# Kernel optimization log

Hardware: AMD Instinct MI355X
Metric: run time of the kernel (lower is better)

Reference implementation:

```python
import jax, jax.numpy as jnp
import numpy as np

N, T, D = 1536, 10, 64
H = 4            # nhead
HD = D // H      # head dim
EPS = 1e-5


def _ln(x, g, b):
    m = x.mean(-1, keepdims=True)
    v = ((x - m) ** 2).mean(-1, keepdims=True)
    return (x - m) / jnp.sqrt(v + EPS) * g + b


def setup_inputs() -> dict:
    key = jax.random.key(0)
    ks = jax.random.split(key, 24)
    s = 0.05
    inp = {
        'trajectories': jax.random.normal(ks[0], (N, T, D), jnp.float32),
        'adj_matrix': jax.random.uniform(ks[1], (N, N), jnp.float32),
        # transformer encoder layer params
        'attn_in_w': jax.random.normal(ks[2], (3 * D, D), jnp.float32) * s,
        'attn_in_b': jnp.zeros((3 * D,), jnp.float32),
        'attn_out_w': jax.random.normal(ks[3], (D, D), jnp.float32) * s,
        'attn_out_b': jnp.zeros((D,), jnp.float32),
        'ln1_g': jnp.ones((D,), jnp.float32),
        'ln1_b': jnp.zeros((D,), jnp.float32),
        'ff_w1': jax.random.normal(ks[4], (64, D), jnp.float32) * s,
        'ff_b1': jnp.zeros((64,), jnp.float32),
        'ff_w2': jax.random.normal(ks[5], (D, 64), jnp.float32) * s,
        'ff_b2': jnp.zeros((D,), jnp.float32),
        'ln2_g': jnp.ones((D,), jnp.float32),
        'ln2_b': jnp.zeros((D,), jnp.float32),
        # 3 GCN layers (hidden 64 -> 64)
        'gcn_w': jax.random.normal(ks[6], (3, 64, 64), jnp.float32) * s,
        'gcn_b': jnp.zeros((3, 64), jnp.float32),
        # edge predictor MLP: (2*64 + T) -> 128 -> 64 -> 1
        'e_w1': jax.random.normal(ks[7], (128, 2 * 64 + T), jnp.float32) * s,
        'e_b1': jnp.zeros((128,), jnp.float32),
        'e_w2': jax.random.normal(ks[8], (64, 128), jnp.float32) * s,
        'e_b2': jnp.zeros((64,), jnp.float32),
        'e_w3': jax.random.normal(ks[9], (1, 64), jnp.float32) * s,
        'e_b3': jnp.zeros((1,), jnp.float32),
    }
    return inp


def reference(trajectories, adj_matrix, attn_in_w, attn_in_b, attn_out_w,
              attn_out_b, ln1_g, ln1_b, ff_w1, ff_b1, ff_w2, ff_b2, ln2_g,
              ln2_b, gcn_w, gcn_b, e_w1, e_b1, e_w2, e_b2, e_w3, e_b3):
    x = trajectories  # (N,T,D)
    # --- torch TransformerEncoderLayer (post-norm, relu, eval mode) ---
    qkv = x @ attn_in_w.T + attn_in_b            # (N,T,3D)
    q, k, v = jnp.split(qkv, 3, axis=-1)
    q = q.reshape(N, T, H, HD)
    k = k.reshape(N, T, H, HD)
    v = v.reshape(N, T, H, HD)
    scores = jnp.einsum('nthd,nshd->nhts', q, k) / jnp.sqrt(jnp.float32(HD))
    attn = jax.nn.softmax(scores, axis=-1)
    ctx = jnp.einsum('nhts,nshd->nthd', attn, v).reshape(N, T, D)
    ctx = ctx @ attn_out_w.T + attn_out_b
    x = _ln(trajectories + ctx, ln1_g, ln1_b)
    ff = jax.nn.relu(x @ ff_w1.T + ff_b1) @ ff_w2.T + ff_b2
    x = _ln(x + ff, ln2_g, ln2_b)
    node = x.mean(axis=1)                        # (N,64)
    # --- GCN stack: relu(linear(adj @ x)) ---
    for l in range(3):
        node = jax.nn.relu((adj_matrix @ node) @ gcn_w[l].T + gcn_b[l])
    # --- vectorized all-pairs edge prediction (i < j) ---
    iu, ju = np.triu_indices(N, k=1)
    iu = jnp.asarray(iu)
    ju = jnp.asarray(ju)
    pair = jnp.concatenate([node[iu], node[ju]], axis=1)       # (P,128)
    diff = trajectories[iu, :, :2] - trajectories[ju, :, :2]   # (P,T,2)
    dist = jnp.sqrt((diff ** 2).sum(-1))                       # (P,T)
    min_dist = dist.min(axis=1)                                # (P,)
    hist = jax.nn.sigmoid(10.0 * (dist - 5.0))                 # (P,T)
    edge = jnp.concatenate([pair, hist], axis=1)               # (P,138)
    h = jax.nn.relu(edge @ e_w1.T + e_b1)
    h = jax.nn.relu(h @ e_w2.T + e_b2)
    prob = jax.nn.sigmoid(h @ e_w3.T + e_b3)[:, 0]             # (P,)
    return prob, min_dist, hist
```

## Files before the change

kernel.cpp:

```cpp
#include <hip/hip_runtime.h>
#include <hip/hip_bf16.h>
#include <math.h>

#define NN 1536
#define TT 10
#define DD 64
#define NHEAD 4
#define HDIM 16
#define PP 1178880

#define WS_W2F   0
#define WS_TXYT  8192
#define WS_GI    38912
#define WS_GJT4  235520
#define WS_NODEA 432128
#define WS_NODEB 530432

using bf16x8 = __attribute__((ext_vector_type(8))) short;
using f32x4  = __attribute__((ext_vector_type(4))) float;

static __device__ __forceinline__ float fsqrt(float x) { return __builtin_amdgcn_sqrtf(x); }
static __device__ __forceinline__ float frcp(float x)  { return __builtin_amdgcn_rcpf(x); }
static __device__ __forceinline__ float fexp(float x)  {
    return __builtin_amdgcn_exp2f(x * 1.44269504088896f);
}
static __device__ __forceinline__ float fsigmoid_neg(float e_arg) {
    return frcp(1.f + fexp(e_arg));
}

static __device__ __forceinline__ unsigned short f2bf_rn(float f) {
    unsigned int u = __float_as_uint(f);
    unsigned int r = (u + 0x7FFFu + ((u >> 16) & 1u)) >> 16;
    return (unsigned short)r;
}
static __device__ __forceinline__ float bf2f(unsigned short h) {
    return __uint_as_float(((unsigned int)h) << 16);
}

static __device__ __forceinline__ float dot64(const float* __restrict__ a,
                                              const float* __restrict__ b) {
    float s = 0.f;
#pragma unroll
    for (int c = 0; c < 64; c += 4) {
        float4 av = *reinterpret_cast<const float4*>(a + c);
        float4 bv = *reinterpret_cast<const float4*>(b + c);
        s = fmaf(av.x, bv.x, s);
        s = fmaf(av.y, bv.y, s);
        s = fmaf(av.z, bv.z, s);
        s = fmaf(av.w, bv.w, s);
    }
    return s;
}

static __device__ __forceinline__ void invert_p(int p, int& io, int& jo) {
    const float Df = (float)((2 * NN - 1) * (2 * NN - 1) - 8 * p);
    int i = (int)(((float)(2 * NN - 1) - fsqrt(Df)) * 0.5f);
    i = i < 0 ? 0 : (i > NN - 2 ? NN - 2 : i);
    while (i * (2 * NN - 1 - i) / 2 > p) --i;
    while ((i + 1) * (2 * NN - 2 - i) / 2 <= p) ++i;
    io = i;
    jo = i + 1 + (p - i * (2 * NN - 1 - i) / 2);
}

#define FMA16(acc, xr, w0, w1, w2, w3)                                   \
    {                                                                    \
        float4 x0 = *reinterpret_cast<const float4*>(xr);                \
        float4 x1 = *reinterpret_cast<const float4*>(xr + 4);            \
        float4 x2 = *reinterpret_cast<const float4*>(xr + 8);            \
        float4 x3 = *reinterpret_cast<const float4*>(xr + 12);           \
        acc = fmaf(x0.x, w0.x, acc); acc = fmaf(x0.y, w0.y, acc);        \
        acc = fmaf(x0.z, w0.z, acc); acc = fmaf(x0.w, w0.w, acc);        \
        acc = fmaf(x1.x, w1.x, acc); acc = fmaf(x1.y, w1.y, acc);        \
        acc = fmaf(x1.z, w1.z, acc); acc = fmaf(x1.w, w1.w, acc);        \
        acc = fmaf(x2.x, w2.x, acc); acc = fmaf(x2.y, w2.y, acc);        \
        acc = fmaf(x2.z, w2.z, acc); acc = fmaf(x2.w, w2.w, acc);        \
        acc = fmaf(x3.x, w3.x, acc); acc = fmaf(x3.y, w3.y, acc);        \
        acc = fmaf(x3.z, w3.z, acc); acc = fmaf(x3.w, w3.w, acc);        \
    }

__global__ __launch_bounds__(128) void k_transformer(
    const float* __restrict__ traj,
    const float* __restrict__ wqkv, const float* __restrict__ bqkv,
    const float* __restrict__ wo,   const float* __restrict__ bo,
    const float* __restrict__ g1,   const float* __restrict__ b1,
    const float* __restrict__ fw1,  const float* __restrict__ fb1,
    const float* __restrict__ fw2,  const float* __restrict__ fb2,
    const float* __restrict__ g2,   const float* __restrict__ b2,
    const float* __restrict__ e_w2,
    float* __restrict__ node_out, unsigned short* __restrict__ w2f,
    float* __restrict__ txyT)
{
    const int bid = blockIdx.x, tid = threadIdx.x;

    if (bid >= NN) {
        const int s = bid - NN;
        if (s < 64) {
#pragma unroll
            for (int q = 0; q < 2; ++q) {
                const int idx = s * 256 + q * 128 + tid;
                int e = idx & 7, lane = (idx >> 3) & 63;
                int half = (idx >> 9) & 1, kk = (idx >> 10) & 3, nt = (idx >> 12) & 3;
                int n = nt * 16 + (lane & 15);
                int k = kk * 32 + (lane >> 4) * 8 + e;
                float v = e_w2[n * 128 + k];
                unsigned short hi = f2bf_rn(v);
                unsigned short lo = f2bf_rn(v - bf2f(hi));
                w2f[idx] = half ? lo : hi;
            }
        } else {
            const int tc = s - 64;
            const int t = tc >> 1, c = tc & 1;
            for (int j = tid; j < NN; j += 128)
                txyT[(size_t)tc * NN + j] = traj[((size_t)j * TT + t) * DD + c];
        }
        return;
    }

    __shared__ __align__(16) float xs[TT][DD];
    __shared__ __align__(16) float qkvs[TT][3 * DD];
    __shared__ __align__(16) float cs[TT][DD];
    __shared__ __align__(16) float ys[TT][DD];
    __shared__ float mv[TT][2];

    const float* xg = traj + (size_t)bid * TT * DD;
    for (int idx = tid; idx < TT * DD; idx += 128)
        xs[idx / DD][idx % DD] = xg[idx];
    __syncthreads();

    {
        float acc[TT];
        const float bq = bqkv[tid];
#pragma unroll
        for (int t = 0; t < TT; ++t) acc[t] = bq;
        const float* wrow = wqkv + (size_t)tid * DD;
#pragma unroll
        for (int c = 0; c < 4; ++c) {
            float4 w0 = *reinterpret_cast<const float4*>(wrow + 16 * c);
            float4 w1 = *reinterpret_cast<const float4*>(wrow + 16 * c + 4);
            float4 w2 = *reinterpret_cast<const float4*>(wrow + 16 * c + 8);
            float4 w3 = *reinterpret_cast<const float4*>(wrow + 16 * c + 12);
#pragma unroll
            for (int t = 0; t < TT; ++t)
                FMA16(acc[t], &xs[t][16 * c], w0, w1, w2, w3);
        }
#pragma unroll
        for (int t = 0; t < TT; ++t) qkvs[t][tid] = acc[t];

        const int o2 = 128 + (tid >> 1);
        const int t0 = (tid & 1) * 5;
        float acc2[5];
        const float bq2 = bqkv[o2];
#pragma unroll
        for (int tt = 0; tt < 5; ++tt) acc2[tt] = bq2;
        const float* wrow2 = wqkv + (size_t)o2 * DD;
#pragma unroll
        for (int c = 0; c < 4; ++c) {
            float4 w0 = *reinterpret_cast<const float4*>(wrow2 + 16 * c);
            float4 w1 = *reinterpret_cast<const float4*>(wrow2 + 16 * c + 4);
            float4 w2 = *reinterpret_cast<const float4*>(wrow2 + 16 * c + 8);
            float4 w3 = *reinterpret_cast<const float4*>(wrow2 + 16 * c + 12);
#pragma unroll
            for (int tt = 0; tt < 5; ++tt)
                FMA16(acc2[tt], &xs[t0 + tt][16 * c], w0, w1, w2, w3);
        }
#pragma unroll
        for (int tt = 0; tt < 5; ++tt) qkvs[t0 + tt][o2] = acc2[tt];
    }
    __syncthreads();

    if (tid < NHEAD * TT) {
        int h = tid / TT, t = tid % TT;
        float sc[TT];
        float mx = -1e30f;
#pragma unroll
        for (int s = 0; s < TT; ++s) {
            float a = 0.f;
#pragma unroll
            for (int d = 0; d < HDIM; ++d)
                a = fmaf(qkvs[t][h * HDIM + d], qkvs[s][DD + h * HDIM + d], a);
            a *= 0.25f;
            sc[s] = a;
            mx = fmaxf(mx, a);
        }
        float den = 0.f;
#pragma unroll
        for (int s = 0; s < TT; ++s) { sc[s] = fexp(sc[s] - mx); den += sc[s]; }
        float inv = frcp(den);
#pragma unroll
        for (int d = 0; d < HDIM; ++d) {
            float a = 0.f;
#pragma unroll
            for (int s = 0; s < TT; ++s)
                a = fmaf(sc[s], qkvs[s][2 * DD + h * HDIM + d], a);
            cs[t][h * HDIM + d] = a * inv;
        }
    }
    __syncthreads();

    {
        const int o = tid & 63, t0 = (tid >> 6) * 5;
        float acc[5];
        const float bv = bo[o];
#pragma unroll
        for (int tt = 0; tt < 5; ++tt) acc[tt] = bv;
        const float* wrow = wo + (size_t)o * DD;
#pragma unroll
        for (int c = 0; c < 4; ++c) {
            float4 w0 = *reinterpret_cast<const float4*>(wrow + 16 * c);
            float4 w1 = *reinterpret_cast<const float4*>(wrow + 16 * c + 4);
            float4 w2 = *reinterpret_cast<const float4*>(wrow + 16 * c + 8);
            float4 w3 = *reinterpret_cast<const float4*>(wrow + 16 * c + 12);
#pragma unroll
            for (int tt = 0; tt < 5; ++tt)
                FMA16(acc[tt], &cs[t0 + tt][16 * c], w0, w1, w2, w3);
        }
#pragma unroll
        for (int tt = 0; tt < 5; ++tt)
            ys[t0 + tt][o] = xs[t0 + tt][o] + acc[tt];
    }
    __syncthreads();

    {
        const int t8 = tid >> 3, s8 = tid & 7;
        if (t8 < TT) {
            const float* yr = &ys[t8][s8 * 8];
            float s1 = 0.f;
#pragma unroll
            for (int c = 0; c < 8; c += 4) {
                float4 v = *reinterpret_cast<const float4*>(yr + c);
                s1 += (v.x + v.y) + (v.z + v.w);
            }
#pragma unroll
            for (int m = 1; m < 8; m <<= 1) s1 += __shfl_xor(s1, m);
            const float mean = s1 * (1.f / DD);
            float s2 = 0.f;
#pragma unroll
            for (int c = 0; c < 8; c += 4) {
                float4 v = *reinterpret_cast<const float4*>(yr + c);
                float d0 = v.x - mean, d1 = v.y - mean, d2 = v.z - mean, d3 = v.w - mean;
                s2 = fmaf(d0, d0, fmaf(d1, d1, fmaf(d2, d2, fmaf(d3, d3, s2))));
            }
#pragma unroll
            for (int m = 1; m < 8; m <<= 1) s2 += __shfl_xor(s2, m);
            if (s8 == 0) {
                mv[t8][0] = mean;
                mv[t8][1] = rsqrtf(s2 * (1.f / DD) + 1e-5f);
            }
        }
    }
    __syncthreads();
    for (int idx = tid; idx < TT * DD; idx += 128) {
        int t = idx / DD, o = idx % DD;
        xs[t][o] = (ys[t][o] - mv[t][0]) * mv[t][1] * g1[o] + b1[o];
    }
    __syncthreads();

    {
        const int pcol = tid & 63, t0 = (tid >> 6) * 5;
        float acc[5];
        const float bv = fb1[pcol];
#pragma unroll
        for (int tt = 0; tt < 5; ++tt) acc[tt] = bv;
        const float* wrow = fw1 + (size_t)pcol * DD;
#pragma unroll
        for (int c = 0; c < 4; ++c) {
            float4 w0 = *reinterpret_cast<const float4*>(wrow + 16 * c);
            float4 w1 = *reinterpret_cast<const float4*>(wrow + 16 * c + 4);
            float4 w2 = *reinterpret_cast<const float4*>(wrow + 16 * c + 8);
            float4 w3 = *reinterpret_cast<const float4*>(wrow + 16 * c + 12);
#pragma unroll
            for (int tt = 0; tt < 5; ++tt)
                FMA16(acc[tt], &xs[t0 + tt][16 * c], w0, w1, w2, w3);
        }
#pragma unroll
        for (int tt = 0; tt < 5; ++tt)
            cs[t0 + tt][pcol] = fmaxf(acc[tt], 0.f);
    }
    __syncthreads();

    {
        const int o = tid & 63, t0 = (tid >> 6) * 5;
        float acc[5];
        const float bv = fb2[o];
#pragma unroll
        for (int tt = 0; tt < 5; ++tt) acc[tt] = bv;
        const float* wrow = fw2 + (size_t)o * DD;
#pragma unroll
        for (int c = 0; c < 4; ++c) {
            float4 w0 = *reinterpret_cast<const float4*>(wrow + 16 * c);
            float4 w1 = *reinterpret_cast<const float4*>(wrow + 16 * c + 4);
            float4 w2 = *reinterpret_cast<const float4*>(wrow + 16 * c + 8);
            float4 w3 = *reinterpret_cast<const float4*>(wrow + 16 * c + 12);
#pragma unroll
            for (int tt = 0; tt < 5; ++tt)
                FMA16(acc[tt], &cs[t0 + tt][16 * c], w0, w1, w2, w3);
        }
#pragma unroll
        for (int tt = 0; tt < 5; ++tt)
            ys[t0 + tt][o] = xs[t0 + tt][o] + acc[tt];
    }
    __syncthreads();

    {
        const int t8 = tid >> 3, s8 = tid & 7;
        if (t8 < TT) {
            const float* yr = &ys[t8][s8 * 8];
            float s1 = 0.f;
#pragma unroll
            for (int c = 0; c < 8; c += 4) {
                float4 v = *reinterpret_cast<const float4*>(yr + c);
                s1 += (v.x + v.y) + (v.z + v.w);
            }
#pragma unroll
            for (int m = 1; m < 8; m <<= 1) s1 += __shfl_xor(s1, m);
            const float mean = s1 * (1.f / DD);
            float s2 = 0.f;
#pragma unroll
            for (int c = 0; c < 8; c += 4) {
                float4 v = *reinterpret_cast<const float4*>(yr + c);
                float d0 = v.x - mean, d1 = v.y - mean, d2 = v.z - mean, d3 = v.w - mean;
                s2 = fmaf(d0, d0, fmaf(d1, d1, fmaf(d2, d2, fmaf(d3, d3, s2))));
            }
#pragma unroll
            for (int m = 1; m < 8; m <<= 1) s2 += __shfl_xor(s2, m);
            if (s8 == 0) {
                mv[t8][0] = mean;
                mv[t8][1] = rsqrtf(s2 * (1.f / DD) + 1e-5f);
            }
        }
    }
    __syncthreads();

    if (tid < DD) {
        float acc = 0.f;
#pragma unroll
        for (int t = 0; t < TT; ++t)
            acc += (ys[t][tid] - mv[t][0]) * mv[t][1];
        node_out[bid * DD + tid] = acc * g2[tid] * (1.f / TT) + b2[tid];
    }
}

__global__ __launch_bounds__(512) void k_gcn(
    const float* __restrict__ A, const float* __restrict__ X,
    const float* __restrict__ W, const float* __restrict__ b,
    float* __restrict__ Y)
{
    __shared__ __align__(16) float part[8][4][68];
    __shared__ __align__(16) float yrow[8][68];
    const int tid = threadIdx.x;
    const int lane = tid & 63;
    const int w = __builtin_amdgcn_readfirstlane(tid >> 6);
    const int rg = w >> 2, jq = w & 3;
    const int i0 = blockIdx.x * 8 + rg * 4;
    const int j0 = jq * (NN / 4);

    const float* a0 = A + (size_t)(i0 + 0) * NN + j0;
    const float* a1 = A + (size_t)(i0 + 1) * NN + j0;
    const float* a2 = A + (size_t)(i0 + 2) * NN + j0;
    const float* a3 = A + (size_t)(i0 + 3) * NN + j0;
    const float* xp = X + (size_t)j0 * 64 + lane;

    float c0 = 0.f, c1 = 0.f, c2 = 0.f, c3 = 0.f;
#pragma unroll 8
    for (int jj = 0; jj < NN / 4; ++jj) {
        const float xv = xp[(size_t)jj * 64];
        c0 = fmaf(a0[jj], xv, c0);
        c1 = fmaf(a1[jj], xv, c1);
        c2 = fmaf(a2[jj], xv, c2);
        c3 = fmaf(a3[jj], xv, c3);
    }
    part[rg * 4 + 0][jq][lane] = c0;
    part[rg * 4 + 1][jq][lane] = c1;
    part[rg * 4 + 2][jq][lane] = c2;
    part[rg * 4 + 3][jq][lane] = c3;
    __syncthreads();

    {
        const int r2 = tid >> 6, o = tid & 63;
        yrow[r2][o] = (part[r2][0][o] + part[r2][1][o])
                    + (part[r2][2][o] + part[r2][3][o]);
    }
    __syncthreads();

    {
        const int r2 = tid >> 6, o = tid & 63;
        float z = b[o] + dot64(&yrow[r2][0], W + o * 64);
        Y[(size_t)(blockIdx.x * 8 + r2) * 64 + o] = fmaxf(z, 0.f);
    }
}

__global__ __launch_bounds__(512) void k_gcn3(
    const float* __restrict__ A, const float* __restrict__ X,
    const float* __restrict__ W, const float* __restrict__ b,
    const float* __restrict__ e_w1, const float* __restrict__ e_b1,
    float* __restrict__ gi_t, float* __restrict__ gjT4)
{
    __shared__ __align__(16) float part[8][4][68];
    __shared__ __align__(16) float yrow[8][68];
    __shared__ __align__(16) float nrow[8][68];
    const int tid = threadIdx.x;
    const int lane = tid & 63;
    const int w = __builtin_amdgcn_readfirstlane(tid >> 6);
    const int rg = w >> 2, jq = w & 3;
    const int i0 = blockIdx.x * 8 + rg * 4;
    const int j0 = jq * (NN / 4);

    const float* a0 = A + (size_t)(i0 + 0) * NN + j0;
    const float* a1 = A + (size_t)(i0 + 1) * NN + j0;
    const float* a2 = A + (size_t)(i0 + 2) * NN + j0;
    const float* a3 = A + (size_t)(i0 + 3) * NN + j0;
    const float* xp = X + (size_t)j0 * 64 + lane;

    float c0 = 0.f, c1 = 0.f, c2 = 0.f, c3 = 0.f;
#pragma unroll 8
    for (int jj = 0; jj < NN / 4; ++jj) {
        const float xv = xp[(size_t)jj * 64];
        c0 = fmaf(a0[jj], xv, c0);
        c1 = fmaf(a1[jj], xv, c1);
        c2 = fmaf(a2[jj], xv, c2);
        c3 = fmaf(a3[jj], xv, c3);
    }
    part[rg * 4 + 0][jq][lane] = c0;
    part[rg * 4 + 1][jq][lane] = c1;
    part[rg * 4 + 2][jq][lane] = c2;
    part[rg * 4 + 3][jq][lane] = c3;
    __syncthreads();

    {
        const int r2 = tid >> 6, o = tid & 63;
        yrow[r2][o] = (part[r2][0][o] + part[r2][1][o])
                    + (part[r2][2][o] + part[r2][3][o]);
    }
    __syncthreads();

    {
        const int r2 = tid >> 6, o = tid & 63;
        float z = b[o] + dot64(&yrow[r2][0], W + o * 64);
        nrow[r2][o] = fmaxf(z, 0.f);
    }
    __syncthreads();

#pragma unroll
    for (int pass = 0; pass < 2; ++pass) {
        const int idx = pass * 512 + tid;
        const int rr = idx >> 7, oo = idx & 127;
        const int i2 = blockIdx.x * 8 + rr;
        gi_t[(size_t)i2 * 128 + oo] = e_b1[oo] + dot64(&nrow[rr][0], e_w1 + oo * 138);
        gjT4[((size_t)(oo >> 2) * NN + i2) * 4 + (oo & 3)] =
            dot64(&nrow[rr][0], e_w1 + oo * 138 + 64);
    }
}

__global__ __launch_bounds__(256, 8) void k_edge(
    const float* __restrict__ txyT,
    const float* __restrict__ gi_t,
    const float* __restrict__ gjT4,
    const float* __restrict__ e_w1,
    const unsigned short* __restrict__ w2f,
    const float* __restrict__ e_b2,
    const float* __restrict__ e_w3, const float* __restrict__ e_b3,
    float* __restrict__ out)
{
    __shared__ __align__(16) unsigned short Ah[64 * 64];
    __shared__ __align__(16) unsigned short Al[64 * 64];
    __shared__ __align__(16) float hs[64][11];
    __shared__ __align__(16) float zsh[4][64];

    const int tid  = threadIdx.x;
    const int lane = tid & 63;
    const int wv   = __builtin_amdgcn_readfirstlane(tid >> 6);
    const int p    = blockIdx.x * 64 + lane;

    int pi, pj;
    invert_p(p, pi, pj);

    {
        float dminp = 3.4e38f;
        for (int t = wv; t < 10; t += 4) {
            float dx = txyT[(size_t)(2 * t) * NN + pi] - txyT[(size_t)(2 * t) * NN + pj];
            float dy = txyT[(size_t)(2 * t + 1) * NN + pi] - txyT[(size_t)(2 * t + 1) * NN + pj];
            float d = fsqrt(fmaf(dx, dx, dy * dy));
            dminp = fminf(dminp, d);
            hs[lane][t] = fsigmoid_neg(50.f - 10.f * d);
        }
        zsh[wv][lane] = dminp;
    }
    __syncthreads();

    float dmin = 0.f;
    if (wv == 0)
        dmin = fminf(fminf(zsh[0][lane], zsh[1][lane]),
                     fminf(zsh[2][lane], zsh[3][lane]));

    float hist[10];
#pragma unroll
    for (int t = 0; t < 10; ++t) hist[t] = hs[lane][t];

    f32x4 acc[4];
#pragma unroll
    for (int pt = 0; pt < 4; ++pt) acc[pt] = (f32x4){0.f, 0.f, 0.f, 0.f};

#pragma unroll
    for (int h = 0; h < 2; ++h) {
        const int ob = h * 64 + wv * 16;
        const float* giRow = gi_t + (size_t)pi * 128 + ob;
        unsigned int ahp[8], alp[8];
#pragma unroll
        for (int q2 = 0; q2 < 4; ++q2) {
            const int o = ob + 4 * q2;
            const float4 gi4 = *reinterpret_cast<const float4*>(giRow + 4 * q2);
            const float4 gj4 = *reinterpret_cast<const float4*>(
                gjT4 + ((size_t)(o >> 2) * NN + pj) * 4);
            float av[4];
#pragma unroll
            for (int k = 0; k < 4; ++k) {
                float a = (&gi4.x)[k] + (&gj4.x)[k];
                const float* wh = e_w1 + (o + k) * 138 + 128;
#pragma unroll
                for (int t = 0; t < 10; ++t) a = fmaf(hist[t], wh[t], a);
                av[k] = fmaxf(a, 0.f);
            }
            const unsigned int u0 = __float_as_uint(av[0]), u1 = __float_as_uint(av[1]);
            const unsigned int u2 = __float_as_uint(av[2]), u3 = __float_as_uint(av[3]);
            ahp[2 * q2]     = __builtin_amdgcn_perm(u1, u0, 0x07060302);
            ahp[2 * q2 + 1] = __builtin_amdgcn_perm(u3, u2, 0x07060302);
            const float l0 = av[0] - __uint_as_float(u0 & 0xFFFF0000u);
            const float l1 = av[1] - __uint_as_float(u1 & 0xFFFF0000u);
            const float l2 = av[2] - __uint_as_float(u2 & 0xFFFF0000u);
            const float l3 = av[3] - __uint_as_float(u3 & 0xFFFF0000u);
            alp[2 * q2]     = __builtin_amdgcn_perm(__float_as_uint(l1), __float_as_uint(l0), 0x07060302);
            alp[2 * q2 + 1] = __builtin_amdgcn_perm(__float_as_uint(l3), __float_as_uint(l2), 0x07060302);
        }

        if (h == 1) __syncthreads();

        char* ahb = (char*)Ah + lane * 128;
        char* alb = (char*)Al + lane * 128;
#pragma unroll
        for (int c = 0; c < 2; ++c) {
            const int boff = ((wv << 5) + (c << 4)) ^ ((lane & 7) << 4);
            *reinterpret_cast<uint4*>(ahb + boff) = *reinterpret_cast<uint4*>(&ahp[4 * c]);
            *reinterpret_cast<uint4*>(alb + boff) = *reinterpret_cast<uint4*>(&alp[4 * c]);
        }

        bf16x8 bh[2], bl[2];
#pragma unroll
        for (int kkl = 0; kkl < 2; ++kkl) {
            const unsigned short* bb =
                w2f + ((size_t)(wv * 4 + 2 * h + kkl) * 2) * 512 + lane * 8;
            bh[kkl] = *reinterpret_cast<const bf16x8*>(bb);
            bl[kkl] = *reinterpret_cast<const bf16x8*>(bb + 512);
        }
        __syncthreads();

        const char* ahr = (const char*)Ah;
        const char* alr = (const char*)Al;
#pragma unroll
        for (int kkl = 0; kkl < 2; ++kkl) {
#pragma unroll
            for (int pt = 0; pt < 4; ++pt) {
                const int row = pt * 16 + (lane & 15);
                const int boff = ((kkl << 6) + ((lane >> 4) << 4)) ^ ((row & 7) << 4);
                bf16x8 afh = *reinterpret_cast<const bf16x8*>(ahr + row * 128 + boff);
                bf16x8 afl = *reinterpret_cast<const bf16x8*>(alr + row * 128 + boff);
                acc[pt] = __builtin_amdgcn_mfma_f32_16x16x32_bf16(afh, bh[kkl], acc[pt], 0, 0, 0);
                acc[pt] = __builtin_amdgcn_mfma_f32_16x16x32_bf16(afh, bl[kkl], acc[pt], 0, 0, 0);
                acc[pt] = __builtin_amdgcn_mfma_f32_16x16x32_bf16(afl, bh[kkl], acc[pt], 0, 0, 0);
            }
        }
    }

    {
        const int m = wv * 16 + (lane & 15);
        const float w3v = e_w3[m];
        const float b2v = e_b2[m];
#pragma unroll
        for (int pt = 0; pt < 4; ++pt) {
            float zs0 = fmaxf(acc[pt][0] + b2v, 0.f) * w3v;
            float zs1 = fmaxf(acc[pt][1] + b2v, 0.f) * w3v;
            float zs2 = fmaxf(acc[pt][2] + b2v, 0.f) * w3v;
            float zs3 = fmaxf(acc[pt][3] + b2v, 0.f) * w3v;
#pragma unroll
            for (int msk = 1; msk < 16; msk <<= 1) {
                zs0 += __shfl_xor(zs0, msk);
                zs1 += __shfl_xor(zs1, msk);
                zs2 += __shfl_xor(zs2, msk);
                zs3 += __shfl_xor(zs3, msk);
            }
            if ((lane & 15) == 0) {
                const int pr = pt * 16 + (lane >> 4) * 4;
                zsh[wv][pr]     = zs0;
                zsh[wv][pr + 1] = zs1;
                zsh[wv][pr + 2] = zs2;
                zsh[wv][pr + 3] = zs3;
            }
        }
    }
    __syncthreads();

    if (wv == 0) {
        float z = zsh[0][lane] + zsh[1][lane] + zsh[2][lane] + zsh[3][lane] + e_b3[0];
        out[p] = fsigmoid_neg(-z);
        out[PP + (size_t)p] = dmin;
    }
    {
        float* hb = out + 2 * (size_t)PP + (size_t)blockIdx.x * 640;
#pragma unroll
        for (int pass = 0; pass < 3; ++pass) {
            const int idx = pass * 256 + tid;
            if (idx < 640)
                hb[idx] = hs[idx / 10][idx % 10];
        }
    }
}

extern "C" void kernel_launch(void* const* d_in, const int* in_sizes, int n_in,
                              void* d_out, int out_size, void* d_ws, size_t ws_size,
                              hipStream_t stream) {
    const float* traj   = (const float*)d_in[0];
    const float* adj    = (const float*)d_in[1];
    const float* w_in   = (const float*)d_in[2];
    const float* b_in   = (const float*)d_in[3];
    const float* w_out  = (const float*)d_in[4];
    const float* b_out  = (const float*)d_in[5];
    const float* ln1g   = (const float*)d_in[6];
    const float* ln1b   = (const float*)d_in[7];
    const float* fw1    = (const float*)d_in[8];
    const float* fb1    = (const float*)d_in[9];
    const float* fw2    = (const float*)d_in[10];
    const float* fb2    = (const float*)d_in[11];
    const float* ln2g   = (const float*)d_in[12];
    const float* ln2b   = (const float*)d_in[13];
    const float* gcn_w  = (const float*)d_in[14];
    const float* gcn_b  = (const float*)d_in[15];
    const float* e_w1   = (const float*)d_in[16];
    const float* e_b1   = (const float*)d_in[17];
    const float* e_w2   = (const float*)d_in[18];
    const float* e_b2   = (const float*)d_in[19];
    const float* e_w3   = (const float*)d_in[20];
    const float* e_b3   = (const float*)d_in[21];

    float* ws    = (float*)d_ws;
    unsigned short* w2f = (unsigned short*)(ws + WS_W2F);
    float* txyT  = ws + WS_TXYT;
    float* gi    = ws + WS_GI;
    float* gjT4  = ws + WS_GJT4;
    float* nodeA = ws + WS_NODEA;
    float* nodeB = ws + WS_NODEB;

    k_transformer<<<NN + 84, 128, 0, stream>>>(traj, w_in, b_in, w_out, b_out,
                                               ln1g, ln1b, fw1, fb1, fw2, fb2,
                                               ln2g, ln2b, e_w2,
                                               nodeA, w2f, txyT);

    k_gcn <<<NN / 8, 512, 0, stream>>>(adj, nodeA, gcn_w,        gcn_b,       nodeB);
    k_gcn <<<NN / 8, 512, 0, stream>>>(adj, nodeB, gcn_w + 4096, gcn_b + 64,  nodeA);
    k_gcn3<<<NN / 8, 512, 0, stream>>>(adj, nodeA, gcn_w + 8192, gcn_b + 128,
                                       e_w1, e_b1, gi, gjT4);

    k_edge<<<PP / 64, 256, 0, stream>>>(txyT, gi, gjT4, e_w1, w2f, e_b2,
                                        e_w3, e_b3, (float*)d_out);
}
```

Before: 234.4 us.

## Split GCN reduction over eight waves per four rows; read transformer input from global

The GCN kernels now give each block 4 output rows, and the 8 waves each cover one eighth of the neighbour dimension. Before, each block handled 8 rows split into 2 groups of 4 waves. This doubles the grid to 384 blocks so more CUs are busy, but each block reads the X matrix once for only 4 rows instead of 8, which cuts reuse. Only half the threads take part in the final reduction and projection. Separately, the QKV projection in the transformer now reads the input rows directly from global memory instead of the staged shared copy, which trades LDS reads for cached global loads.

```diff
diff --git a/kernel.cpp b/kernel.cpp
--- a/kernel.cpp
+++ b/kernel.cpp
@@ -141,7 +141,7 @@
             float4 w3 = *reinterpret_cast<const float4*>(wrow + 16 * c + 12);
 #pragma unroll
             for (int t = 0; t < TT; ++t)
-                FMA16(acc[t], &xs[t][16 * c], w0, w1, w2, w3);
+                FMA16(acc[t], xg + t * DD + 16 * c, w0, w1, w2, w3);
         }
 #pragma unroll
         for (int t = 0; t < TT; ++t) qkvs[t][tid] = acc[t];
@@ -345,14 +345,13 @@
     const float* __restrict__ W, const float* __restrict__ b,
     float* __restrict__ Y)
 {
-    __shared__ __align__(16) float part[8][4][68];
-    __shared__ __align__(16) float yrow[8][68];
+    __shared__ __align__(16) float part[4][8][68];
+    __shared__ __align__(16) float yrow[4][68];
     const int tid = threadIdx.x;
     const int lane = tid & 63;
     const int w = __builtin_amdgcn_readfirstlane(tid >> 6);
-    const int rg = w >> 2, jq = w & 3;
-    const int i0 = blockIdx.x * 8 + rg * 4;
-    const int j0 = jq * (NN / 4);
+    const int i0 = blockIdx.x * 4;
+    const int j0 = w * (NN / 8);
 
     const float* a0 = A + (size_t)(i0 + 0) * NN + j0;
     const float* a1 = A + (size_t)(i0 + 1) * NN + j0;
@@ -362,30 +361,32 @@
 
     float c0 = 0.f, c1 = 0.f, c2 = 0.f, c3 = 0.f;
 #pragma unroll 8
-    for (int jj = 0; jj < NN / 4; ++jj) {
+    for (int jj = 0; jj < NN / 8; ++jj) {
         const float xv = xp[(size_t)jj * 64];
         c0 = fmaf(a0[jj], xv, c0);
         c1 = fmaf(a1[jj], xv, c1);
         c2 = fmaf(a2[jj], xv, c2);
         c3 = fmaf(a3[jj], xv, c3);
     }
-    part[rg * 4 + 0][jq][lane] = c0;
-    part[rg * 4 + 1][jq][lane] = c1;
-    part[rg * 4 + 2][jq][lane] = c2;
-    part[rg * 4 + 3][jq][lane] = c3;
-    __syncthreads();
-
-    {
+    part[0][w][lane] = c0;
+    part[1][w][lane] = c1;
+    part[2][w][lane] = c2;
+    part[3][w][lane] = c3;
+    __syncthreads();
+
+    if (tid < 256) {
         const int r2 = tid >> 6, o = tid & 63;
-        yrow[r2][o] = (part[r2][0][o] + part[r2][1][o])
-                    + (part[r2][2][o] + part[r2][3][o]);
-    }
-    __syncthreads();
-
-    {
+        float s = 0.f;
+#pragma unroll
+        for (int k = 0; k < 8; ++k) s += part[r2][k][o];
+        yrow[r2][o] = s;
+    }
+    __syncthreads();
+
+    if (tid < 256) {
         const int r2 = tid >> 6, o = tid & 63;
         float z = b[o] + dot64(&yrow[r2][0], W + o * 64);
-        Y[(size_t)(blockIdx.x * 8 + r2) * 64 + o] = fmaxf(z, 0.f);
+        Y[(size_t)(i0 + r2) * 64 + o] = fmaxf(z, 0.f);
     }
 }
 
@@ -395,15 +396,14 @@
     const float* __restrict__ e_w1, const float* __restrict__ e_b1,
     float* __restrict__ gi_t, float* __restrict__ gjT4)
 {
-    __shared__ __align__(16) float part[8][4][68];
-    __shared__ __align__(16) float yrow[8][68];
-    __shared__ __align__(16) float nrow[8][68];
+    __shared__ __align__(16) float part[4][8][68];
+    __shared__ __align__(16) float yrow[4][68];
+    __shared__ __align__(16) float nrow[4][68];
     const int tid = threadIdx.x;
     const int lane = tid & 63;
     const int w = __builtin_amdgcn_readfirstlane(tid >> 6);
-    const int rg = w >> 2, jq = w & 3;
-    const int i0 = blockIdx.x * 8 + rg * 4;
-    const int j0 = jq * (NN / 4);
+    const int i0 = blockIdx.x * 4;
+    const int j0 = w * (NN / 8);
 
     const float* a0 = A + (size_t)(i0 + 0) * NN + j0;
     const float* a1 = A + (size_t)(i0 + 1) * NN + j0;
@@ -413,38 +413,39 @@
 
     float c0 = 0.f, c1 = 0.f, c2 = 0.f, c3 = 0.f;
 #pragma unroll 8
-    for (int jj = 0; jj < NN / 4; ++jj) {
+    for (int jj = 0; jj < NN / 8; ++jj) {
         const float xv = xp[(size_t)jj * 64];
         c0 = fmaf(a0[jj], xv, c0);
         c1 = fmaf(a1[jj], xv, c1);
         c2 = fmaf(a2[jj], xv, c2);
         c3 = fmaf(a3[jj], xv, c3);
     }
-    part[rg * 4 + 0][jq][lane] = c0;
-    part[rg * 4 + 1][jq][lane] = c1;
-    part[rg * 4 + 2][jq][lane] = c2;
-    part[rg * 4 + 3][jq][lane] = c3;
-    __syncthreads();
-
-    {
+    part[0][w][lane] = c0;
+    part[1][w][lane] = c1;
+    part[2][w][lane] = c2;
+    part[3][w][lane] = c3;
+    __syncthreads();
+
+    if (tid < 256) {
         const int r2 = tid >> 6, o = tid & 63;
-        yrow[r2][o] = (part[r2][0][o] + part[r2][1][o])
-                    + (part[r2][2][o] + part[r2][3][o]);
-    }
-    __syncthreads();
-
-    {
+        float s = 0.f;
+#pragma unroll
+        for (int k = 0; k < 8; ++k) s += part[r2][k][o];
+        yrow[r2][o] = s;
+    }
+    __syncthreads();
+
+    if (tid < 256) {
         const int r2 = tid >> 6, o = tid & 63;
         float z = b[o] + dot64(&yrow[r2][0], W + o * 64);
         nrow[r2][o] = fmaxf(z, 0.f);
     }
     __syncthreads();
 
-#pragma unroll
-    for (int pass = 0; pass < 2; ++pass) {
-        const int idx = pass * 512 + tid;
-        const int rr = idx >> 7, oo = idx & 127;
-        const int i2 = blockIdx.x * 8 + rr;
+    {
+        const int rr = tid >> 7;
+        const int oo = tid & 127;
+        const int i2 = i0 + rr;
         gi_t[(size_t)i2 * 128 + oo] = e_b1[oo] + dot64(&nrow[rr][0], e_w1 + oo * 138);
         gjT4[((size_t)(oo >> 2) * NN + i2) * 4 + (oo & 3)] =
             dot64(&nrow[rr][0], e_w1 + oo * 138 + 64);
@@ -653,9 +654,9 @@
                                                ln2g, ln2b, e_w2,
                                                nodeA, w2f, txyT);
 
-    k_gcn <<<NN / 8, 512, 0, stream>>>(adj, nodeA, gcn_w,        gcn_b,       nodeB);
-    k_gcn <<<NN / 8, 512, 0, stream>>>(adj, nodeB, gcn_w + 4096, gcn_b + 64,  nodeA);
-    k_gcn3<<<NN / 8, 512, 0, stream>>>(adj, nodeA, gcn_w + 8192, gcn_b + 128,
+    k_gcn <<<NN / 4, 512, 0, stream>>>(adj, nodeA, gcn_w,        gcn_b,       nodeB);
+    k_gcn <<<NN / 4, 512, 0, stream>>>(adj, nodeB, gcn_w + 4096, gcn_b + 64,  nodeA);
+    k_gcn3<<<NN / 4, 512, 0, stream>>>(adj, nodeA, gcn_w + 8192, gcn_b + 128,
                                        e_w1, e_b1, gi, gjT4);
 
     k_edge<<<PP / 64, 256, 0, stream>>>(txyT, gi, gjT4, e_w1, w2f, e_b2,
```

New measurement: 220.5 us. -5.9%, faster.
